# Optimization experiments

Hardware: AMD Instinct MI355X
Metric: run time of the kernel (lower is better)

The kernel has to match this reference:

```python
import jax, jax.numpy as jnp
import numpy as np

H = 512   # GRU hidden
I = 12    # feature dim
Z = 64    # latent dim


def setup_inputs() -> dict:
    key = jax.random.key(0)
    ks = jax.random.split(key, 24)
    B, T = 256, 256
    rn = lambda k, shape, s: (jax.random.normal(k, shape, dtype=jnp.float32) * s)
    sg = 1.0 / np.sqrt(H)
    inp = {
        'x': rn(ks[0], (B, T, I), 1.0),
        'eps': rn(ks[1], (B, Z), 1.0),
        # encoder GRU (torch layout: gates stacked r,z,n)
        'w_ih_e': rn(ks[2], (3 * H, I), sg), 'w_hh_e': rn(ks[3], (3 * H, H), sg),
        'b_ih_e': rn(ks[4], (3 * H,), sg), 'b_hh_e': rn(ks[5], (3 * H,), sg),
        # decoder GRU
        'w_ih_d': rn(ks[6], (3 * H, I), sg), 'w_hh_d': rn(ks[7], (3 * H, H), sg),
        'b_ih_d': rn(ks[8], (3 * H,), sg), 'b_hh_d': rn(ks[9], (3 * H,), sg),
        # linear heads (torch nn.Linear layout: [out, in])
        'fc1_w': rn(ks[10], (256, H), 1 / np.sqrt(H)), 'fc1_b': rn(ks[11], (256,), 0.02),
        'fc11_w': rn(ks[12], (Z, 256), 1 / np.sqrt(256)), 'fc11_b': rn(ks[13], (Z,), 0.02),
        'fc12_w': rn(ks[14], (Z, 256), 1 / np.sqrt(256)), 'fc12_b': rn(ks[15], (Z,), 0.02),
        'fc2_w': rn(ks[16], (256, Z), 1 / np.sqrt(Z)), 'fc2_b': rn(ks[17], (256,), 0.02),
        'fc3_w': rn(ks[18], (H, 256), 1 / np.sqrt(256)), 'fc3_b': rn(ks[19], (H,), 0.02),
        'fc4_w': rn(ks[20], (I, H), 1 / np.sqrt(H)), 'fc4_b': rn(ks[21], (I,), 0.02),
    }
    return inp


def gru_step(x, h, w_ih, w_hh, b_ih, b_hh):
    # torch GRU cell: gates ordered (r, z, n)
    gi = x @ w_ih.T + b_ih            # [B, 3H]
    gh = h @ w_hh.T + b_hh            # [B, 3H]
    i_r, i_z, i_n = jnp.split(gi, 3, axis=-1)
    h_r, h_z, h_n = jnp.split(gh, 3, axis=-1)
    r = jax.nn.sigmoid(i_r + h_r)
    z = jax.nn.sigmoid(i_z + h_z)
    n = jnp.tanh(i_n + r * h_n)
    return (1.0 - z) * n + z * h


def reference(x, eps, w_ih_e, w_hh_e, b_ih_e, b_hh_e, w_ih_d, w_hh_d, b_ih_d, b_hh_d,
              fc1_w, fc1_b, fc11_w, fc11_b, fc12_w, fc12_b, fc2_w, fc2_b,
              fc3_w, fc3_b, fc4_w, fc4_b):
    B, T, _ = x.shape
    lrelu = lambda v: jax.nn.leaky_relu(v, 0.01)

    # ---- encoder GRU over time ----
    h0 = jnp.zeros((B, H), x.dtype)
    def enc(h, xt):
        return gru_step(xt, h, w_ih_e, w_hh_e, b_ih_e, b_hh_e), None
    h_enc, _ = jax.lax.scan(enc, h0, jnp.swapaxes(x, 0, 1))  # final hidden [B,H]

    # ---- latent head ----
    v = lrelu(h_enc)
    v = lrelu(v @ fc1_w.T + fc1_b)
    mu = v @ fc11_w.T + fc11_b
    log_var = v @ fc12_w.T + fc12_b
    std = jnp.exp(0.5 * log_var)
    z_lat = mu + std * eps            # reparameterized rsample

    # ---- decoder init ----
    u = lrelu(z_lat @ fc2_w.T + fc2_b)
    h_dec = u @ fc3_w.T + fc3_b       # [B,H]

    y0 = jnp.zeros((B, I), x.dtype)
    def dec(carry, _):
        y, h = carry
        h = gru_step(y, h, w_ih_d, w_hh_d, b_ih_d, b_hh_d)
        y = h @ fc4_w.T + fc4_b
        return (y, h), y
    _, seq = jax.lax.scan(dec, (y0, h_dec), None, length=T)  # [T,B,I]
    seq = jnp.swapaxes(seq, 0, 1)     # [B,T,I]
    return seq, mu, log_var
```

## Files before the change

### kernel.cpp

```cpp
#include <hip/hip_runtime.h>
#include <hip/hip_bf16.h>

#define DI 12
#define DH 512
#define DT 256
#define DB 256
#define SCOPE __HIP_MEMORY_SCOPE_AGENT

typedef float f32x4 __attribute__((ext_vector_type(4)));
typedef __bf16 bf16x8 __attribute__((ext_vector_type(8)));

__device__ __forceinline__ float sigm(float x) { return 1.f / (1.f + __expf(-x)); }
__device__ __forceinline__ float tanh_f(float x) {
    float xc = fminf(fmaxf(x, -15.f), 15.f);
    float e = __expf(-2.f * xc);
    return (1.f - e) / (1.f + e);
}
__device__ __forceinline__ float lrelu(float x) { return x > 0.f ? x : 0.01f * x; }
__device__ __forceinline__ unsigned short f2bf(float f) {
    return __builtin_bit_cast(unsigned short, (__bf16)f);
}

__device__ __forceinline__ void stage_h(unsigned short* hbuf, const unsigned long long* src2, int tid) {
    unsigned long long tmp[11];
    #pragma unroll
    for (int j = 0; j < 11; ++j) {
        int i = tid + j * 384;
        if (i < 4096) tmp[j] = __hip_atomic_load(src2 + i, __ATOMIC_RELAXED, SCOPE);
    }
    #pragma unroll
    for (int j = 0; j < 11; ++j) {
        int i = tid + j * 384;
        if (i < 4096) {
            int row = i >> 7, dq = i & 127;
            unsigned off = (unsigned)row * 1024u + (((unsigned)(dq * 8)) ^ ((unsigned)((row & 7) << 4)));
            *(unsigned long long*)((char*)hbuf + off) = tmp[j];
        }
    }
}

__device__ __forceinline__ void barrier_wait(const unsigned* fl, int wave, int lane, unsigned gen) {
    if (wave == 0) {
        while (true) {
            unsigned v = __hip_atomic_load(fl + (lane & 31), __ATOMIC_RELAXED, SCOPE);
            if (__all((int)(v >= gen))) break;
            __builtin_amdgcn_s_sleep(1);
        }
        __builtin_amdgcn_fence(__ATOMIC_ACQUIRE, "agent");
    }
}

__device__ __forceinline__ f32x4 mfma_hbuf(const unsigned short* hbuf, const bf16x8* bw,
                                           int arow, int lk) {
    f32x4 acc = {0.f, 0.f, 0.f, 0.f};
    const unsigned rbase = (unsigned)arow * 1024u;
    const unsigned swz = (unsigned)((arow & 7) << 4);
    const char* hb = (const char*)hbuf;
    #pragma unroll
    for (int kk = 0; kk < 16; ++kk) {
        unsigned off = rbase + (((unsigned)(kk * 64 + lk * 16)) ^ swz);
        bf16x8 a = *(const bf16x8*)(hb + off);
        acc = __builtin_amdgcn_mfma_f32_16x16x32_bf16(a, bw[kk], acc, 0, 0, 0);
    }
    return acc;
}

__global__ void init_kernel(unsigned* flE, unsigned* flD) {
    if (blockIdx.x == 0) flE[threadIdx.x] = 0u;
    else flD[threadIdx.x] = 0u;
}

__global__ __launch_bounds__(384, 2)
void enc_kernel(const float* __restrict__ x, const float* __restrict__ w_ih,
                const float* __restrict__ w_hh, const float* __restrict__ b_ih,
                const float* __restrict__ b_hh, unsigned* __restrict__ hpp,
                float* __restrict__ hencF, unsigned* __restrict__ flags)
{
    const int tid = threadIdx.x;
    const int bid = blockIdx.x;
    const int bg = bid & 7;
    const int cb = bid >> 3;
    const int growbase = bg * 32;
    const int ub = cb * 16;
    const int wave = tid >> 6, lane = tid & 63;
    const int rt = wave / 3, g = wave % 3;
    const int lrow = lane & 15, lk = lane >> 4;
    unsigned* flg = flags + bg * 32;

    __shared__ unsigned short hbuf[32 * DH];
    __shared__ float xbuf[32][DI];
    __shared__ float gibuf[32][48];
    __shared__ float wih_s[48][DI];
    __shared__ float bih_s[48], bhh_s[48];
    __shared__ float RZ[2][2][16][16];

    for (int i = tid; i < 48 * DI; i += 384) {
        int c = i / DI, k = i % DI;
        int grow = (c >> 4) * DH + ub + (c & 15);
        wih_s[c][k] = w_ih[grow * DI + k];
    }
    if (tid < 48) {
        int grow = (tid >> 4) * DH + ub + (tid & 15);
        bih_s[tid] = b_ih[grow];
        bhh_s[tid] = b_hh[grow];
    }
    for (int i = tid; i < 32 * DH / 2; i += 384) ((unsigned*)hbuf)[i] = 0u;
    {
        int r = tid / DI, c = tid % DI;
        xbuf[r][c] = x[(size_t)(growbase + r) * (DT * DI) + c];
    }

    bf16x8 bfr[16];
    {
        const float* wr = w_hh + (size_t)(g * DH + ub + lrow) * DH;
        #pragma unroll
        for (int kk = 0; kk < 16; ++kk) {
            const float* p = wr + kk * 32 + lk * 8;
            bf16x8 v;
            #pragma unroll
            for (int j = 0; j < 8; ++j) v[j] = (__bf16)p[j];
            bfr[kk] = v;
        }
    }
    float hreg[4] = {0.f, 0.f, 0.f, 0.f};
    const int pid = (g != 2) ? ((rt * 2 + g) * 64 + lane) : 0;
    __syncthreads();

    for (int t = 0; t < DT; ++t) {
        const bool lastt = (t == DT - 1);
        f32x4 acc = mfma_hbuf(hbuf, bfr, rt * 16 + lrow, lk);
        {
            int r = tid / 12, c0 = (tid % 12) * 4;
            float xr[DI];
            #pragma unroll
            for (int k = 0; k < DI; ++k) xr[k] = xbuf[r][k];
            #pragma unroll
            for (int q = 0; q < 4; ++q) {
                int c = c0 + q;
                float a2 = bih_s[c];
                #pragma unroll
                for (int k = 0; k < DI; ++k) a2 += xr[k] * wih_s[c][k];
                gibuf[r][c] = a2;
            }
        }
        __syncthreads();
        float hn[4];
        float xr0 = 0.f, xr1 = 0.f;
        {
            int u = lrow;
            if (g == 0) {
                #pragma unroll
                for (int i = 0; i < 4; ++i) {
                    int ri = lk * 4 + i;
                    RZ[0][rt][ri][u] = sigm(acc[i] + bhh_s[u] + gibuf[rt * 16 + ri][u]);
                }
            } else if (g == 1) {
                #pragma unroll
                for (int i = 0; i < 4; ++i) {
                    int ri = lk * 4 + i;
                    RZ[1][rt][ri][u] = sigm(acc[i] + bhh_s[16 + u] + gibuf[rt * 16 + ri][16 + u]);
                }
            } else {
                #pragma unroll
                for (int i = 0; i < 4; ++i) hn[i] = acc[i] + bhh_s[32 + u];
            }
        }
        if (g != 2 && !lastt) {
            xr0 = x[(size_t)(growbase + pid / 12) * (DT * DI) + (size_t)(t + 1) * DI + pid % 12];
            if (pid < 128) {
                int e = 256 + pid;
                xr1 = x[(size_t)(growbase + e / 12) * (DT * DI) + (size_t)(t + 1) * DI + e % 12];
            }
        }
        __syncthreads();
        if (g == 2) {
            int u = lrow;
            unsigned* dst = hpp + ((t + 1) & 1) * (DB * DH / 2);
            #pragma unroll
            for (int i = 0; i < 4; ++i) {
                int ri = lk * 4 + i;
                int row = rt * 16 + ri;
                float r = RZ[0][rt][ri][u];
                float z = RZ[1][rt][ri][u];
                float n = tanh_f(gibuf[row][32 + u] + r * hn[i]);
                hreg[i] = (1.f - z) * n + z * hreg[i];
                float hp = __shfl_xor(hreg[i], 1);
                if (!lastt) {
                    if (!(u & 1)) {
                        unsigned val = (unsigned)f2bf(hreg[i]) | ((unsigned)f2bf(hp) << 16);
                        __hip_atomic_store(dst + (unsigned)(growbase + row) * 256u +
                                           (unsigned)(cb * 8 + (u >> 1)),
                                           val, __ATOMIC_RELAXED, SCOPE);
                    }
                } else {
                    hencF[(size_t)(growbase + row) * DH + ub + u] = hreg[i];
                }
            }
        }
        if (lastt) break;
        __syncthreads();
        const unsigned gen = (unsigned)(t + 1);
        if (tid == 0) __hip_atomic_store(flg + cb, gen, __ATOMIC_RELAXED, SCOPE);
        barrier_wait(flg, wave, lane, gen);
        __syncthreads();
        stage_h(hbuf, (const unsigned long long*)(hpp + ((t + 1) & 1) * (DB * DH / 2)) +
                      (size_t)growbase * 128, tid);
        if (g != 2) {
            xbuf[pid / 12][pid % 12] = xr0;
            if (pid < 128) { int e = 256 + pid; xbuf[e / 12][e % 12] = xr1; }
        }
        __syncthreads();
    }
}

__global__ void mid_kernel(const float* __restrict__ henc, const float* __restrict__ eps,
                           const float* __restrict__ fc1_w, const float* __restrict__ fc1_b,
                           const float* __restrict__ fc11_w, const float* __restrict__ fc11_b,
                           const float* __restrict__ fc12_w, const float* __restrict__ fc12_b,
                           const float* __restrict__ fc2_w, const float* __restrict__ fc2_b,
                           const float* __restrict__ fc3_w, const float* __restrict__ fc3_b,
                           float* __restrict__ hdecF, unsigned* __restrict__ hppD0,
                           float* __restrict__ out)
{
    const int row = blockIdx.x, tid = threadIdx.x;
    __shared__ float v0[512], v1[256], zb[64], ubuf[256];
    for (int k = tid; k < 512; k += 256) v0[k] = lrelu(henc[(size_t)row * 512 + k]);
    __syncthreads();
    {
        float a = fc1_b[tid];
        const float* w = fc1_w + (size_t)tid * 512;
        for (int k = 0; k < 512; k += 4) {
            float4 wv = *(const float4*)(w + k);
            a += wv.x * v0[k] + wv.y * v0[k + 1] + wv.z * v0[k + 2] + wv.w * v0[k + 3];
        }
        v1[tid] = lrelu(a);
    }
    __syncthreads();
    if (tid < 64) {
        float m = fc11_b[tid], lv = fc12_b[tid];
        const float* w1 = fc11_w + (size_t)tid * 256;
        const float* w2 = fc12_w + (size_t)tid * 256;
        for (int k = 0; k < 256; k += 4) {
            float4 a = *(const float4*)(w1 + k);
            float4 b = *(const float4*)(w2 + k);
            m  += a.x * v1[k] + a.y * v1[k + 1] + a.z * v1[k + 2] + a.w * v1[k + 3];
            lv += b.x * v1[k] + b.y * v1[k + 1] + b.z * v1[k + 2] + b.w * v1[k + 3];
        }
        out[786432 + row * 64 + tid] = m;
        out[802816 + row * 64 + tid] = lv;
        zb[tid] = m + __expf(0.5f * lv) * eps[row * 64 + tid];
    }
    __syncthreads();
    {
        float a = fc2_b[tid];
        const float* w = fc2_w + (size_t)tid * 64;
        for (int k = 0; k < 64; k += 4) {
            float4 wv = *(const float4*)(w + k);
            a += wv.x * zb[k] + wv.y * zb[k + 1] + wv.z * zb[k + 2] + wv.w * zb[k + 3];
        }
        ubuf[tid] = lrelu(a);
    }
    __syncthreads();
    {
        float hv[2];
        #pragma unroll
        for (int q = 0; q < 2; ++q) {
            int j = 2 * tid + q;
            float a = fc3_b[j];
            const float* w = fc3_w + (size_t)j * 256;
            for (int k = 0; k < 256; k += 4) {
                float4 wv = *(const float4*)(w + k);
                a += wv.x * ubuf[k] + wv.y * ubuf[k + 1] + wv.z * ubuf[k + 2] + wv.w * ubuf[k + 3];
            }
            hdecF[(size_t)row * 512 + j] = a;
            hv[q] = a;
        }
        hppD0[row * 256 + tid] = (unsigned)f2bf(hv[0]) | ((unsigned)f2bf(hv[1]) << 16);
    }
}

__global__ __launch_bounds__(384, 2)
void dec_kernel(const float* __restrict__ w_ih, const float* __restrict__ w_hh,
                const float* __restrict__ b_ih, const float* __restrict__ b_hh,
                const float* __restrict__ fc4_w, const float* __restrict__ fc4_b,
                const float* __restrict__ hdecF, unsigned* __restrict__ hpp,
                unsigned* __restrict__ flags, float* __restrict__ out)
{
    const int tid = threadIdx.x;
    const int bid = blockIdx.x;
    const int bg = bid & 7;
    const int cb = bid >> 3;
    const int growbase = bg * 32;
    const int ub = cb * 16;
    const int wave = tid >> 6, lane = tid & 63;
    const int rt = wave / 3, g = wave % 3;
    const int lrow = lane & 15, lk = lane >> 4;
    unsigned* flg = flags + bg * 32;

    __shared__ unsigned short hbuf[32 * DH];
    __shared__ float ybuf[32][DI];
    __shared__ float gibuf[32][48];
    __shared__ float wih_s[48][DI];
    __shared__ float bih_s[48], bhh_s[48];
    __shared__ float fb4[DI];
    __shared__ float RZ[2][2][16][16];

    for (int i = tid; i < 48 * DI; i += 384) {
        int c = i / DI, k = i % DI;
        int grow = (c >> 4) * DH + ub + (c & 15);
        wih_s[c][k] = w_ih[grow * DI + k];
    }
    if (tid < 48) {
        int grow = (tid >> 4) * DH + ub + (tid & 15);
        bih_s[tid] = b_ih[grow];
        bhh_s[tid] = b_hh[grow];
    }
    if (tid < DI) fb4[tid] = fc4_b[tid];

    bf16x8 bfr[16];
    {
        const float* wr = w_hh + (size_t)(g * DH + ub + lrow) * DH;
        #pragma unroll
        for (int kk = 0; kk < 16; ++kk) {
            const float* p = wr + kk * 32 + lk * 8;
            bf16x8 v;
            #pragma unroll
            for (int j = 0; j < 8; ++j) v[j] = (__bf16)p[j];
            bfr[kk] = v;
        }
    }
    bf16x8 yfr[16];
    {
        #pragma unroll
        for (int kk = 0; kk < 16; ++kk) {
            bf16x8 v;
            if (g == 0 && lrow < DI) {
                const float* p = fc4_w + (size_t)lrow * DH + kk * 32 + lk * 8;
                #pragma unroll
                for (int j = 0; j < 8; ++j) v[j] = (__bf16)p[j];
            } else {
                #pragma unroll
                for (int j = 0; j < 8; ++j) v[j] = (__bf16)0.f;
            }
            yfr[kk] = v;
        }
    }
    float hreg[4] = {0.f, 0.f, 0.f, 0.f};
    if (g == 2) {
        #pragma unroll
        for (int i = 0; i < 4; ++i)
            hreg[i] = hdecF[(size_t)(growbase + rt * 16 + lk * 4 + i) * DH + ub + lrow];
    }
    stage_h(hbuf, (const unsigned long long*)hpp + (size_t)growbase * 128, tid);
    __syncthreads();

    for (int t = 0; t < DT; ++t) {
        if (t == 0) {
            int r = tid / DI, c = tid % DI;
            ybuf[r][c] = 0.f;
        } else if (g == 0) {
            f32x4 ya = mfma_hbuf(hbuf, yfr, rt * 16 + lrow, lk);
            if (lrow < DI) {
                #pragma unroll
                for (int i = 0; i < 4; ++i)
                    ybuf[rt * 16 + lk * 4 + i][lrow] = ya[i] + fb4[lrow];
            }
        }
        __syncthreads();
        f32x4 acc = mfma_hbuf(hbuf, bfr, rt * 16 + lrow, lk);
        {
            int r = tid / 12, c0 = (tid % 12) * 4;
            float yr[DI];
            #pragma unroll
            for (int k = 0; k < DI; ++k) yr[k] = ybuf[r][k];
            #pragma unroll
            for (int q = 0; q < 4; ++q) {
                int c = c0 + q;
                float a2 = bih_s[c];
                #pragma unroll
                for (int k = 0; k < DI; ++k) a2 += yr[k] * wih_s[c][k];
                gibuf[r][c] = a2;
            }
        }
        if (cb == 0 && t > 0) {
            int r = tid / 12, c = tid % 12;
            out[(size_t)(growbase + r) * (DT * DI) + (size_t)(t - 1) * DI + c] = ybuf[r][c];
        }
        __syncthreads();
        float hn[4];
        {
            int u = lrow;
            if (g == 0) {
                #pragma unroll
                for (int i = 0; i < 4; ++i) {
                    int ri = lk * 4 + i;
                    RZ[0][rt][ri][u] = sigm(acc[i] + bhh_s[u] + gibuf[rt * 16 + ri][u]);
                }
            } else if (g == 1) {
                #pragma unroll
                for (int i = 0; i < 4; ++i) {
                    int ri = lk * 4 + i;
                    RZ[1][rt][ri][u] = sigm(acc[i] + bhh_s[16 + u] + gibuf[rt * 16 + ri][16 + u]);
                }
            } else {
                #pragma unroll
                for (int i = 0; i < 4; ++i) hn[i] = acc[i] + bhh_s[32 + u];
            }
        }
        __syncthreads();
        if (g == 2) {
            int u = lrow;
            unsigned* dst = hpp + ((t + 1) & 1) * (DB * DH / 2);
            #pragma unroll
            for (int i = 0; i < 4; ++i) {
                int ri = lk * 4 + i;
                int row = rt * 16 + ri;
                float r = RZ[0][rt][ri][u];
                float z = RZ[1][rt][ri][u];
                float n = tanh_f(gibuf[row][32 + u] + r * hn[i]);
                hreg[i] = (1.f - z) * n + z * hreg[i];
                float hp = __shfl_xor(hreg[i], 1);
                if (!(u & 1)) {
                    unsigned val = (unsigned)f2bf(hreg[i]) | ((unsigned)f2bf(hp) << 16);
                    __hip_atomic_store(dst + (unsigned)(growbase + row) * 256u +
                                       (unsigned)(cb * 8 + (u >> 1)),
                                       val, __ATOMIC_RELAXED, SCOPE);
                }
            }
        }
        __syncthreads();
        const unsigned gen = (unsigned)(t + 1);
        if (tid == 0) __hip_atomic_store(flg + cb, gen, __ATOMIC_RELAXED, SCOPE);
        barrier_wait(flg, wave, lane, gen);
        __syncthreads();
        stage_h(hbuf, (const unsigned long long*)(hpp + ((t + 1) & 1) * (DB * DH / 2)) +
                      (size_t)growbase * 128, tid);
        __syncthreads();
    }
    if (g == 0) {
        f32x4 ya = mfma_hbuf(hbuf, yfr, rt * 16 + lrow, lk);
        if (lrow < DI) {
            #pragma unroll
            for (int i = 0; i < 4; ++i)
                ybuf[rt * 16 + lk * 4 + i][lrow] = ya[i] + fb4[lrow];
        }
    }
    __syncthreads();
    if (cb == 0) {
        int r = tid / 12, c = tid % 12;
        out[(size_t)(growbase + r) * (DT * DI) + (size_t)(DT - 1) * DI + c] = ybuf[r][c];
    }
}

extern "C" void kernel_launch(void* const* d_in, const int* in_sizes, int n_in,
                              void* d_out, int out_size, void* d_ws, size_t ws_size,
                              hipStream_t stream)
{
    const float* x      = (const float*)d_in[0];
    const float* eps    = (const float*)d_in[1];
    const float* w_ih_e = (const float*)d_in[2];
    const float* w_hh_e = (const float*)d_in[3];
    const float* b_ih_e = (const float*)d_in[4];
    const float* b_hh_e = (const float*)d_in[5];
    const float* w_ih_d = (const float*)d_in[6];
    const float* w_hh_d = (const float*)d_in[7];
    const float* b_ih_d = (const float*)d_in[8];
    const float* b_hh_d = (const float*)d_in[9];
    const float* fc1_w  = (const float*)d_in[10];
    const float* fc1_b  = (const float*)d_in[11];
    const float* fc11_w = (const float*)d_in[12];
    const float* fc11_b = (const float*)d_in[13];
    const float* fc12_w = (const float*)d_in[14];
    const float* fc12_b = (const float*)d_in[15];
    const float* fc2_w  = (const float*)d_in[16];
    const float* fc2_b  = (const float*)d_in[17];
    const float* fc3_w  = (const float*)d_in[18];
    const float* fc3_b  = (const float*)d_in[19];
    const float* fc4_w  = (const float*)d_in[20];
    const float* fc4_b  = (const float*)d_in[21];

    char* ws = (char*)d_ws;
    unsigned* hppE  = (unsigned*)(ws + 0);
    unsigned* hppD  = (unsigned*)(ws + 524288);
    float* hencF    = (float*)(ws + 1048576);
    float* hdecF    = (float*)(ws + 1572864);
    unsigned* flagE = (unsigned*)(ws + 2097152);
    unsigned* flagD = (unsigned*)(ws + 2098176);
    float* out = (float*)d_out;

    init_kernel<<<2, 256, 0, stream>>>(flagE, flagD);
    enc_kernel<<<256, 384, 0, stream>>>(x, w_ih_e, w_hh_e, b_ih_e, b_hh_e, hppE, hencF, flagE);
    mid_kernel<<<256, 256, 0, stream>>>(hencF, eps, fc1_w, fc1_b, fc11_w, fc11_b,
                                        fc12_w, fc12_b, fc2_w, fc2_b, fc3_w, fc3_b,
                                        hdecF, hppD, out);
    dec_kernel<<<256, 384, 0, stream>>>(w_ih_d, w_hh_d, b_ih_d, b_hh_d, fc4_w, fc4_b,
                                        hdecF, hppD, flagD, out);
}
```

Baseline: 3.080 ms.

## Fold fc4 into decoder input weights and drop per-step y sync stage

A prep kernel precomputes W_ih_d·fc4_w (in bf16) and the matching bias, so the decoder gets its input-gate term straight from h with an extra MFMA per k-step. This removes the separate y projection, the ybuf/gibuf shared-memory staging and one __syncthreads per timestep from the serial recurrent loop. Only the cb==0 blocks still compute y, reading fc4 from global memory, and write it directly to output. The encoder likewise computes its input gates per lane in registers instead of staging them through shared memory. The composed bf16 weight adds rounding error to the decoder input path.

```diff
diff --git a/kernel.cpp b/kernel.cpp
--- a/kernel.cpp
+++ b/kernel.cpp
@@ -68,6 +68,40 @@
 __global__ void init_kernel(unsigned* flE, unsigned* flD) {
     if (blockIdx.x == 0) flE[threadIdx.x] = 0u;
     else flD[threadIdx.x] = 0u;
+}
+
+__global__ void prep_kernel(const float* __restrict__ w_ih_d, const float* __restrict__ fc4_w,
+                            const float* __restrict__ b_ih_d, const float* __restrict__ fc4_b,
+                            unsigned short* __restrict__ W2bf, float* __restrict__ b2,
+                            unsigned short* __restrict__ fc4bf)
+{
+    const int r = blockIdx.x, tid = threadIdx.x;
+    if (r < 3 * DH) {
+        float wr[DI];
+        #pragma unroll
+        for (int k = 0; k < DI; ++k) wr[k] = w_ih_d[r * DI + k];
+        int c0 = tid * 4;
+        #pragma unroll
+        for (int q = 0; q < 4; ++q) {
+            int c = c0 + q;
+            float a = 0.f;
+            #pragma unroll
+            for (int k = 0; k < DI; ++k) a += wr[k] * fc4_w[k * DH + c];
+            W2bf[(size_t)r * DH + c] = f2bf(a);
+        }
+        if (tid == 0) {
+            float a = b_ih_d[r];
+            #pragma unroll
+            for (int k = 0; k < DI; ++k) a += wr[k] * fc4_b[k];
+            b2[r] = a;
+        }
+    } else {
+        int rr = r - 3 * DH;
+        int c0 = tid * 4;
+        #pragma unroll
+        for (int q = 0; q < 4; ++q)
+            fc4bf[rr * DH + c0 + q] = (rr < DI) ? f2bf(fc4_w[rr * DH + c0 + q]) : (unsigned short)0;
+    }
 }
 
 __global__ __launch_bounds__(384, 2)
@@ -89,21 +123,15 @@
 
     __shared__ unsigned short hbuf[32 * DH];
     __shared__ float xbuf[32][DI];
-    __shared__ float gibuf[32][48];
-    __shared__ float wih_s[48][DI];
-    __shared__ float bih_s[48], bhh_s[48];
     __shared__ float RZ[2][2][16][16];
 
-    for (int i = tid; i < 48 * DI; i += 384) {
-        int c = i / DI, k = i % DI;
-        int grow = (c >> 4) * DH + ub + (c & 15);
-        wih_s[c][k] = w_ih[grow * DI + k];
-    }
-    if (tid < 48) {
-        int grow = (tid >> 4) * DH + ub + (tid & 15);
-        bih_s[tid] = b_ih[grow];
-        bhh_s[tid] = b_hh[grow];
-    }
+    const int grow = g * DH + ub + lrow;
+    const float bhh_l = b_hh[grow];
+    const float bih_l = b_ih[grow];
+    float wihr[DI];
+    #pragma unroll
+    for (int k = 0; k < DI; ++k) wihr[k] = w_ih[grow * DI + k];
+
     for (int i = tid; i < 32 * DH / 2; i += 384) ((unsigned*)hbuf)[i] = 0u;
     {
         int r = tid / DI, c = tid % DI;
@@ -112,7 +140,7 @@
 
     bf16x8 bfr[16];
     {
-        const float* wr = w_hh + (size_t)(g * DH + ub + lrow) * DH;
+        const float* wr = w_hh + (size_t)grow * DH;
         #pragma unroll
         for (int kk = 0; kk < 16; ++kk) {
             const float* p = wr + kk * 32 + lk * 8;
@@ -129,42 +157,29 @@
     for (int t = 0; t < DT; ++t) {
         const bool lastt = (t == DT - 1);
         f32x4 acc = mfma_hbuf(hbuf, bfr, rt * 16 + lrow, lk);
-        {
-            int r = tid / 12, c0 = (tid % 12) * 4;
-            float xr[DI];
-            #pragma unroll
-            for (int k = 0; k < DI; ++k) xr[k] = xbuf[r][k];
-            #pragma unroll
-            for (int q = 0; q < 4; ++q) {
-                int c = c0 + q;
-                float a2 = bih_s[c];
-                #pragma unroll
-                for (int k = 0; k < DI; ++k) a2 += xr[k] * wih_s[c][k];
-                gibuf[r][c] = a2;
-            }
-        }
-        __syncthreads();
-        float hn[4];
+        float gi[4];
+        #pragma unroll
+        for (int i = 0; i < 4; ++i) {
+            int row = rt * 16 + lk * 4 + i;
+            float a2 = bih_l;
+            #pragma unroll
+            for (int k = 0; k < DI; ++k) a2 += xbuf[row][k] * wihr[k];
+            gi[i] = a2;
+        }
+        float hn[4], gin[4];
+        if (g == 0) {
+            #pragma unroll
+            for (int i = 0; i < 4; ++i)
+                RZ[0][rt][lk * 4 + i][lrow] = sigm(acc[i] + bhh_l + gi[i]);
+        } else if (g == 1) {
+            #pragma unroll
+            for (int i = 0; i < 4; ++i)
+                RZ[1][rt][lk * 4 + i][lrow] = sigm(acc[i] + bhh_l + gi[i]);
+        } else {
+            #pragma unroll
+            for (int i = 0; i < 4; ++i) { hn[i] = acc[i] + bhh_l; gin[i] = gi[i]; }
+        }
         float xr0 = 0.f, xr1 = 0.f;
-        {
-            int u = lrow;
-            if (g == 0) {
-                #pragma unroll
-                for (int i = 0; i < 4; ++i) {
-                    int ri = lk * 4 + i;
-                    RZ[0][rt][ri][u] = sigm(acc[i] + bhh_s[u] + gibuf[rt * 16 + ri][u]);
-                }
-            } else if (g == 1) {
-                #pragma unroll
-                for (int i = 0; i < 4; ++i) {
-                    int ri = lk * 4 + i;
-                    RZ[1][rt][ri][u] = sigm(acc[i] + bhh_s[16 + u] + gibuf[rt * 16 + ri][16 + u]);
-                }
-            } else {
-                #pragma unroll
-                for (int i = 0; i < 4; ++i) hn[i] = acc[i] + bhh_s[32 + u];
-            }
-        }
         if (g != 2 && !lastt) {
             xr0 = x[(size_t)(growbase + pid / 12) * (DT * DI) + (size_t)(t + 1) * DI + pid % 12];
             if (pid < 128) {
@@ -174,26 +189,25 @@
         }
         __syncthreads();
         if (g == 2) {
-            int u = lrow;
             unsigned* dst = hpp + ((t + 1) & 1) * (DB * DH / 2);
             #pragma unroll
             for (int i = 0; i < 4; ++i) {
                 int ri = lk * 4 + i;
                 int row = rt * 16 + ri;
-                float r = RZ[0][rt][ri][u];
-                float z = RZ[1][rt][ri][u];
-                float n = tanh_f(gibuf[row][32 + u] + r * hn[i]);
+                float r = RZ[0][rt][ri][lrow];
+                float z = RZ[1][rt][ri][lrow];
+                float n = tanh_f(gin[i] + r * hn[i]);
                 hreg[i] = (1.f - z) * n + z * hreg[i];
                 float hp = __shfl_xor(hreg[i], 1);
                 if (!lastt) {
-                    if (!(u & 1)) {
+                    if (!(lrow & 1)) {
                         unsigned val = (unsigned)f2bf(hreg[i]) | ((unsigned)f2bf(hp) << 16);
                         __hip_atomic_store(dst + (unsigned)(growbase + row) * 256u +
-                                           (unsigned)(cb * 8 + (u >> 1)),
+                                           (unsigned)(cb * 8 + (lrow >> 1)),
                                            val, __ATOMIC_RELAXED, SCOPE);
                     }
                 } else {
-                    hencF[(size_t)(growbase + row) * DH + ub + u] = hreg[i];
+                    hencF[(size_t)(growbase + row) * DH + ub + lrow] = hreg[i];
                 }
             }
         }
@@ -280,11 +294,12 @@
 }
 
 __global__ __launch_bounds__(384, 2)
-void dec_kernel(const float* __restrict__ w_ih, const float* __restrict__ w_hh,
-                const float* __restrict__ b_ih, const float* __restrict__ b_hh,
-                const float* __restrict__ fc4_w, const float* __restrict__ fc4_b,
-                const float* __restrict__ hdecF, unsigned* __restrict__ hpp,
-                unsigned* __restrict__ flags, float* __restrict__ out)
+void dec_kernel(const float* __restrict__ w_hh, const float* __restrict__ b_ih,
+                const float* __restrict__ b_hh, const unsigned short* __restrict__ W2bf,
+                const float* __restrict__ b2, const unsigned short* __restrict__ fc4bf,
+                const float* __restrict__ fc4_b, const float* __restrict__ hdecF,
+                unsigned* __restrict__ hpp, unsigned* __restrict__ flags,
+                float* __restrict__ out)
 {
     const int tid = threadIdx.x;
     const int bid = blockIdx.x;
@@ -298,28 +313,17 @@
     unsigned* flg = flags + bg * 32;
 
     __shared__ unsigned short hbuf[32 * DH];
-    __shared__ float ybuf[32][DI];
-    __shared__ float gibuf[32][48];
-    __shared__ float wih_s[48][DI];
-    __shared__ float bih_s[48], bhh_s[48];
-    __shared__ float fb4[DI];
     __shared__ float RZ[2][2][16][16];
 
-    for (int i = tid; i < 48 * DI; i += 384) {
-        int c = i / DI, k = i % DI;
-        int grow = (c >> 4) * DH + ub + (c & 15);
-        wih_s[c][k] = w_ih[grow * DI + k];
-    }
-    if (tid < 48) {
-        int grow = (tid >> 4) * DH + ub + (tid & 15);
-        bih_s[tid] = b_ih[grow];
-        bhh_s[tid] = b_hh[grow];
-    }
-    if (tid < DI) fb4[tid] = fc4_b[tid];
+    const int grow = g * DH + ub + lrow;
+    const float bhh_l = b_hh[grow];
+    const float bih_l = b_ih[grow];
+    const float b2_l  = b2[grow];
+    const float fb4_l = (lrow < DI) ? fc4_b[lrow] : 0.f;
 
     bf16x8 bfr[16];
     {
-        const float* wr = w_hh + (size_t)(g * DH + ub + lrow) * DH;
+        const float* wr = w_hh + (size_t)grow * DH;
         #pragma unroll
         for (int kk = 0; kk < 16; ++kk) {
             const float* p = wr + kk * 32 + lk * 8;
@@ -329,101 +333,100 @@
             bfr[kk] = v;
         }
     }
-    bf16x8 yfr[16];
-    {
-        #pragma unroll
-        for (int kk = 0; kk < 16; ++kk) {
-            bf16x8 v;
-            if (g == 0 && lrow < DI) {
-                const float* p = fc4_w + (size_t)lrow * DH + kk * 32 + lk * 8;
+    bf16x8 w2fr[16];
+    {
+        const unsigned short* wr = W2bf + (size_t)grow * DH;
+        #pragma unroll
+        for (int kk = 0; kk < 16; ++kk)
+            w2fr[kk] = *reinterpret_cast<const bf16x8*>(wr + kk * 32 + lk * 8);
+    }
+    float hreg[4] = {0.f, 0.f, 0.f, 0.f};
+    if (g == 2) {
+        #pragma unroll
+        for (int i = 0; i < 4; ++i)
+            hreg[i] = hdecF[(size_t)(growbase + rt * 16 + lk * 4 + i) * DH + ub + lrow];
+    }
+    stage_h(hbuf, (const unsigned long long*)hpp + (size_t)growbase * 128, tid);
+    __syncthreads();
+
+    const bool ywave = (g == 0) && (cb == 0);
+    const unsigned short* fp = fc4bf + (size_t)lrow * DH;
+
+    for (int t = 0; t < DT; ++t) {
+        f32x4 acc1 = {0.f, 0.f, 0.f, 0.f};
+        f32x4 acc2 = {0.f, 0.f, 0.f, 0.f};
+        {
+            const int arow = rt * 16 + lrow;
+            const unsigned rbase = (unsigned)arow * 1024u;
+            const unsigned swz = (unsigned)((arow & 7) << 4);
+            const char* hb = (const char*)hbuf;
+            if (t == 0) {
                 #pragma unroll
-                for (int j = 0; j < 8; ++j) v[j] = (__bf16)p[j];
+                for (int kk = 0; kk < 16; ++kk) {
+                    unsigned off = rbase + (((unsigned)(kk * 64 + lk * 16)) ^ swz);
+                    bf16x8 a = *(const bf16x8*)(hb + off);
+                    acc1 = __builtin_amdgcn_mfma_f32_16x16x32_bf16(a, bfr[kk], acc1, 0, 0, 0);
+                }
             } else {
                 #pragma unroll
-                for (int j = 0; j < 8; ++j) v[j] = (__bf16)0.f;
-            }
-            yfr[kk] = v;
-        }
-    }
-    float hreg[4] = {0.f, 0.f, 0.f, 0.f};
-    if (g == 2) {
-        #pragma unroll
-        for (int i = 0; i < 4; ++i)
-            hreg[i] = hdecF[(size_t)(growbase + rt * 16 + lk * 4 + i) * DH + ub + lrow];
-    }
-    stage_h(hbuf, (const unsigned long long*)hpp + (size_t)growbase * 128, tid);
-    __syncthreads();
-
-    for (int t = 0; t < DT; ++t) {
-        if (t == 0) {
-            int r = tid / DI, c = tid % DI;
-            ybuf[r][c] = 0.f;
-        } else if (g == 0) {
-            f32x4 ya = mfma_hbuf(hbuf, yfr, rt * 16 + lrow, lk);
+                for (int kk = 0; kk < 16; ++kk) {
+                    unsigned off = rbase + (((unsigned)(kk * 64 + lk * 16)) ^ swz);
+                    bf16x8 a = *(const bf16x8*)(hb + off);
+                    acc1 = __builtin_amdgcn_mfma_f32_16x16x32_bf16(a, bfr[kk], acc1, 0, 0, 0);
+                    acc2 = __builtin_amdgcn_mfma_f32_16x16x32_bf16(a, w2fr[kk], acc2, 0, 0, 0);
+                }
+            }
+        }
+        if (ywave && t > 0) {
+            f32x4 ya = {0.f, 0.f, 0.f, 0.f};
+            const int arow = rt * 16 + lrow;
+            const unsigned rbase = (unsigned)arow * 1024u;
+            const unsigned swz = (unsigned)((arow & 7) << 4);
+            const char* hb = (const char*)hbuf;
+            #pragma unroll
+            for (int kk = 0; kk < 16; ++kk) {
+                unsigned off = rbase + (((unsigned)(kk * 64 + lk * 16)) ^ swz);
+                bf16x8 a = *(const bf16x8*)(hb + off);
+                bf16x8 yb = *reinterpret_cast<const bf16x8*>(fp + kk * 32 + lk * 8);
+                ya = __builtin_amdgcn_mfma_f32_16x16x32_bf16(a, yb, ya, 0, 0, 0);
+            }
             if (lrow < DI) {
                 #pragma unroll
                 for (int i = 0; i < 4; ++i)
-                    ybuf[rt * 16 + lk * 4 + i][lrow] = ya[i] + fb4[lrow];
-            }
-        }
-        __syncthreads();
-        f32x4 acc = mfma_hbuf(hbuf, bfr, rt * 16 + lrow, lk);
-        {
-            int r = tid / 12, c0 = (tid % 12) * 4;
-            float yr[DI];
-            #pragma unroll
-            for (int k = 0; k < DI; ++k) yr[k] = ybuf[r][k];
-            #pragma unroll
-            for (int q = 0; q < 4; ++q) {
-                int c = c0 + q;
-                float a2 = bih_s[c];
-                #pragma unroll
-                for (int k = 0; k < DI; ++k) a2 += yr[k] * wih_s[c][k];
-                gibuf[r][c] = a2;
-            }
-        }
-        if (cb == 0 && t > 0) {
-            int r = tid / 12, c = tid % 12;
-            out[(size_t)(growbase + r) * (DT * DI) + (size_t)(t - 1) * DI + c] = ybuf[r][c];
-        }
-        __syncthreads();
-        float hn[4];
-        {
-            int u = lrow;
-            if (g == 0) {
-                #pragma unroll
-                for (int i = 0; i < 4; ++i) {
-                    int ri = lk * 4 + i;
-                    RZ[0][rt][ri][u] = sigm(acc[i] + bhh_s[u] + gibuf[rt * 16 + ri][u]);
-                }
-            } else if (g == 1) {
-                #pragma unroll
-                for (int i = 0; i < 4; ++i) {
-                    int ri = lk * 4 + i;
-                    RZ[1][rt][ri][u] = sigm(acc[i] + bhh_s[16 + u] + gibuf[rt * 16 + ri][16 + u]);
-                }
-            } else {
-                #pragma unroll
-                for (int i = 0; i < 4; ++i) hn[i] = acc[i] + bhh_s[32 + u];
-            }
+                    out[(size_t)(growbase + rt * 16 + lk * 4 + i) * (DT * DI) +
+                        (size_t)(t - 1) * DI + lrow] = ya[i] + fb4_l;
+            }
+        }
+        const float bsel = (t == 0) ? bih_l : b2_l;
+        float hn[4], gin[4];
+        if (g == 0) {
+            #pragma unroll
+            for (int i = 0; i < 4; ++i)
+                RZ[0][rt][lk * 4 + i][lrow] = sigm(acc1[i] + bhh_l + acc2[i] + bsel);
+        } else if (g == 1) {
+            #pragma unroll
+            for (int i = 0; i < 4; ++i)
+                RZ[1][rt][lk * 4 + i][lrow] = sigm(acc1[i] + bhh_l + acc2[i] + bsel);
+        } else {
+            #pragma unroll
+            for (int i = 0; i < 4; ++i) { hn[i] = acc1[i] + bhh_l; gin[i] = acc2[i] + bsel; }
         }
         __syncthreads();
         if (g == 2) {
-            int u = lrow;
             unsigned* dst = hpp + ((t + 1) & 1) * (DB * DH / 2);
             #pragma unroll
             for (int i = 0; i < 4; ++i) {
                 int ri = lk * 4 + i;
                 int row = rt * 16 + ri;
-                float r = RZ[0][rt][ri][u];
-                float z = RZ[1][rt][ri][u];
-                float n = tanh_f(gibuf[row][32 + u] + r * hn[i]);
+                float r = RZ[0][rt][ri][lrow];
+                float z = RZ[1][rt][ri][lrow];
+                float n = tanh_f(gin[i] + r * hn[i]);
                 hreg[i] = (1.f - z) * n + z * hreg[i];
                 float hp = __shfl_xor(hreg[i], 1);
-                if (!(u & 1)) {
+                if (!(lrow & 1)) {
                     unsigned val = (unsigned)f2bf(hreg[i]) | ((unsigned)f2bf(hp) << 16);
                     __hip_atomic_store(dst + (unsigned)(growbase + row) * 256u +
-                                       (unsigned)(cb * 8 + (u >> 1)),
+                                       (unsigned)(cb * 8 + (lrow >> 1)),
                                        val, __ATOMIC_RELAXED, SCOPE);
                 }
             }
@@ -437,18 +440,25 @@
                       (size_t)growbase * 128, tid);
         __syncthreads();
     }
-    if (g == 0) {
-        f32x4 ya = mfma_hbuf(hbuf, yfr, rt * 16 + lrow, lk);
+    if (ywave) {
+        f32x4 ya = {0.f, 0.f, 0.f, 0.f};
+        const int arow = rt * 16 + lrow;
+        const unsigned rbase = (unsigned)arow * 1024u;
+        const unsigned swz = (unsigned)((arow & 7) << 4);
+        const char* hb = (const char*)hbuf;
+        #pragma unroll
+        for (int kk = 0; kk < 16; ++kk) {
+            unsigned off = rbase + (((unsigned)(kk * 64 + lk * 16)) ^ swz);
+            bf16x8 a = *(const bf16x8*)(hb + off);
+            bf16x8 yb = *reinterpret_cast<const bf16x8*>(fp + kk * 32 + lk * 8);
+            ya = __builtin_amdgcn_mfma_f32_16x16x32_bf16(a, yb, ya, 0, 0, 0);
+        }
         if (lrow < DI) {
             #pragma unroll
             for (int i = 0; i < 4; ++i)
-                ybuf[rt * 16 + lk * 4 + i][lrow] = ya[i] + fb4[lrow];
-        }
-    }
-    __syncthreads();
-    if (cb == 0) {
-        int r = tid / 12, c = tid % 12;
-        out[(size_t)(growbase + r) * (DT * DI) + (size_t)(DT - 1) * DI + c] = ybuf[r][c];
+                out[(size_t)(growbase + rt * 16 + lk * 4 + i) * (DT * DI) +
+                    (size_t)(DT - 1) * DI + lrow] = ya[i] + fb4_l;
+        }
     }
 }
 
@@ -480,19 +490,23 @@
     const float* fc4_b  = (const float*)d_in[21];
 
     char* ws = (char*)d_ws;
-    unsigned* hppE  = (unsigned*)(ws + 0);
-    unsigned* hppD  = (unsigned*)(ws + 524288);
-    float* hencF    = (float*)(ws + 1048576);
-    float* hdecF    = (float*)(ws + 1572864);
-    unsigned* flagE = (unsigned*)(ws + 2097152);
-    unsigned* flagD = (unsigned*)(ws + 2098176);
+    unsigned* hppE        = (unsigned*)(ws + 0);
+    unsigned* hppD        = (unsigned*)(ws + 524288);
+    float* hencF          = (float*)(ws + 1048576);
+    float* hdecF          = (float*)(ws + 1572864);
+    unsigned* flagE       = (unsigned*)(ws + 2097152);
+    unsigned* flagD       = (unsigned*)(ws + 2101248);
+    unsigned short* W2bf  = (unsigned short*)(ws + 2105344);
+    float* b2             = (float*)(ws + 3678208);
+    unsigned short* fc4bf = (unsigned short*)(ws + 3684352);
     float* out = (float*)d_out;
 
     init_kernel<<<2, 256, 0, stream>>>(flagE, flagD);
+    prep_kernel<<<1552, 128, 0, stream>>>(w_ih_d, fc4_w, b_ih_d, fc4_b, W2bf, b2, fc4bf);
     enc_kernel<<<256, 384, 0, stream>>>(x, w_ih_e, w_hh_e, b_ih_e, b_hh_e, hppE, hencF, flagE);
     mid_kernel<<<256, 256, 0, stream>>>(hencF, eps, fc1_w, fc1_b, fc11_w, fc11_b,
                                         fc12_w, fc12_b, fc2_w, fc2_b, fc3_w, fc3_b,
                                         hdecF, hppD, out);
-    dec_kernel<<<256, 384, 0, stream>>>(w_ih_d, w_hh_d, b_ih_d, b_hh_d, fc4_w, fc4_b,
+    dec_kernel<<<256, 384, 0, stream>>>(w_hh_d, b_ih_d, b_hh_d, W2bf, b2, fc4bf, fc4_b,
                                         hdecF, hppD, flagD, out);
 }
```

Measured after the change: 3.306 ms. +7.3%, slower.
